# Performance work log

Measured on AMD Instinct MI355X. Metric: run time of the kernel, lower is better.

Reference implementation:

```python
import jax, jax.numpy as jnp
import numpy as np

EMBED_DIM_LIST = [256, 512]
NUM_HEADS_LIST = [4, 8]
MAX_EMBED = 512
N_BASE = 8                       # = max(num_heads_list)
MAX_HS = max(EMBED_DIM_LIST) // min(NUM_HEADS_LIST)  # 128


def _config_masks():
    # One {0,1} mask per (emb, heads) config, shape [n_cfg, N_BASE, MAX_HS, MAX_EMBED].
    # Mask encodes: slice base weight [:head_size, :emb], zero-pad to (MAX_HS, MAX_EMBED),
    # and that only the first `heads` base heads receive a contribution.
    r = np.arange(MAX_HS)[:, None]
    c = np.arange(MAX_EMBED)[None, :]
    masks = []
    for emb in EMBED_DIM_LIST:
        for heads in NUM_HEADS_LIST:
            hs = emb // heads
            m2 = ((r < hs) & (c < emb)).astype(np.float32)      # [MAX_HS, MAX_EMBED]
            hm = (np.arange(N_BASE) < heads).astype(np.float32)  # [N_BASE]
            masks.append(hm[:, None, None] * m2[None])
    return jnp.asarray(np.stack(masks))  # [4, 8, 128, 512]

_CFG_MASKS = _config_masks()


def setup_inputs() -> dict:
    key = jax.random.key(0)
    k0, k1, k2, k3, k4 = jax.random.split(key, 5)
    B, T = 4, 2048
    x = jax.random.normal(k0, (B, T, MAX_EMBED), dtype=jnp.float32)
    weights = jax.random.uniform(k1, (len(EMBED_DIM_LIST) * len(NUM_HEADS_LIST),), dtype=jnp.float32)
    s = 0.02
    base_K = jax.random.normal(k2, (N_BASE, MAX_HS, MAX_EMBED), dtype=jnp.float32) * s
    base_Q = jax.random.normal(k3, (N_BASE, MAX_HS, MAX_EMBED), dtype=jnp.float32) * s
    base_V = jax.random.normal(k4, (N_BASE, MAX_HS, MAX_EMBED), dtype=jnp.float32) * s
    return {"x": x, "weights": weights, "base_K": base_K, "base_Q": base_Q, "base_V": base_V}


def reference(x, weights, base_K, base_Q, base_V):
    B, T, C = x.shape
    # Weight mixing: sum_i weights[i] * (padded slice of base weight) for each base head.
    eff = jnp.einsum('i,ihde->hde', weights, _CFG_MASKS)  # [H, MAX_HS, MAX_EMBED]
    Wk = eff * base_K
    Wq = eff * base_Q
    Wv = eff * base_V
    # Projections for all base heads at once: F.linear(x, W) == x @ W.T
    k = jnp.einsum('btc,hdc->bhtd', x, Wk)
    q = jnp.einsum('btc,hdc->bhtd', x, Wq)
    v = jnp.einsum('btc,hdc->bhtd', x, Wv)
    # Causal self-attention; scale uses k.shape[-1] == MAX_HS (padded head size), as in source.
    scale = 1.0 / jnp.sqrt(jnp.asarray(MAX_HS, dtype=x.dtype))
    att = jnp.einsum('bhtd,bhsd->bhts', q, k) * scale       # [B, H, T, T]
    tril = jnp.tril(jnp.ones((T, T), dtype=bool))
    att = jnp.where(tril, att, -jnp.inf)
    wei = jax.nn.softmax(att, axis=-1)                       # dropout = identity (eval)
    out = jnp.einsum('bhts,bhsd->bhtd', wei, v)              # [B, H, T, MAX_HS]
    # torch.cat(head_out_list, dim=-1) in head order == transpose + reshape
    return out.transpose(0, 2, 1, 3).reshape(B, T, N_BASE * MAX_HS)
```

## Files before the change

### kernel.cpp

```cpp
#include <hip/hip_runtime.h>
#include <hip/hip_bf16.h>
#include <stdint.h>

typedef __attribute__((ext_vector_type(8))) short bf16x8;
typedef __attribute__((ext_vector_type(4))) float f32x4;
typedef __attribute__((ext_vector_type(16))) float f32x16;

#define MFMA16(a,b,c) __builtin_amdgcn_mfma_f32_16x16x32_bf16((a),(b),(c),0,0,0)
#define MFMA32(a,b,c) __builtin_amdgcn_mfma_f32_32x32x16_bf16((a),(b),(c),0,0,0)
#define AS1 __attribute__((address_space(1)))
#define AS3 __attribute__((address_space(3)))

__device__ inline short f2bf(float f) {
    union { __hip_bfloat16 h; short s; } u;
    u.h = __float2bfloat16(f);
    return u.s;
}
__device__ inline uint32_t pack_bf16(float a, float b) {
    union { __hip_bfloat16 h; uint16_t u; } ua, ub;
    ua.h = __float2bfloat16(a); ub.h = __float2bfloat16(b);
    return (uint32_t)ua.u | ((uint32_t)ub.u << 16);
}

#if __has_builtin(__builtin_amdgcn_permlane32_swap)
#define SWAP32(x, y, a, b) { auto _r = __builtin_amdgcn_permlane32_swap((a),(b),false,false); \
                             (x) = _r[0]; (y) = _r[1]; }
#else
#define SWAP32(x, y, a, b) { uint32_t _ta = __shfl_xor((uint32_t)(a),32); \
                             uint32_t _tb = __shfl_xor((uint32_t)(b),32); \
                             (x) = hh_ ? _tb : (a); (y) = hh_ ? (b) : _ta; }
#endif

#define QSCALE 0.12751879523879295f

#define NW (8*128*512)
#define NWC (768*512)
#define NX4 (8192*512/4)
#define NZ1 262144

__global__ void prep_kernel(const float* __restrict__ x,
                            const float* __restrict__ w,
                            const float* __restrict__ bK,
                            const float* __restrict__ bQ,
                            const float* __restrict__ bV,
                            short* __restrict__ xb,
                            short* __restrict__ W,
                            short* __restrict__ qkv)
{
    const float w0 = w[0], w1 = w[1], w2 = w[2], w3 = w[3];
    const size_t HSTRIDE = (size_t)2048 * 128;
    const uint4 zz = {0u, 0u, 0u, 0u};
    for (int i = blockIdx.x * blockDim.x + threadIdx.x; i < NW + NX4 + 3 * NZ1;
         i += gridDim.x * blockDim.x) {
        if (i < NW) {
            int e = i & 511;
            int d = (i >> 9) & 127;
            int h = i >> 16;
            if (h >= 4 && d >= 64) continue;
            float eff = 0.f;
            if (h < 4) { eff += w2; if (d < 64 && e < 256) eff += w0; }
            if (d < 32 && e < 256) eff += w1;
            if (d < 64) eff += w3;
            int r = (h < 4) ? (h * 128 + d) : (512 + (h - 4) * 64 + d);
            int idx = r * 512 + e;
            W[idx]           = f2bf(eff * bK[i]);
            W[idx + NWC]     = f2bf(eff * bQ[i] * QSCALE);
            W[idx + 2*NWC]   = f2bf(eff * bV[i]);
        } else if (i < NW + NX4) {
            int j = i - NW;
            float4 v = ((const float4*)x)[j];
            short4 o;
            o.x = f2bf(v.x); o.y = f2bf(v.y); o.z = f2bf(v.z); o.w = f2bf(v.w);
            ((short4*)xb)[j] = o;
        } else {
            int z = i - NW - NX4;
            int reg = z / NZ1;
            int zz_ = z - reg * NZ1;
            int bhidx = zz_ >> 14;
            int rem = zz_ & 16383;
            int bh = (bhidx >> 2) * 8 + 4 + (bhidx & 3);
            short* p;
            if (reg < 2) {
                int t = rem >> 3, ch = rem & 7;
                p = qkv + (size_t)reg * 32 * HSTRIDE + (size_t)bh * HSTRIDE
                    + (size_t)t * 128 + 64 + ch * 8;
            } else {
                p = qkv + (size_t)64 * HSTRIDE + (size_t)bh * HSTRIDE
                    + (size_t)64 * 2048 + (size_t)rem * 8;
            }
            *(uint4*)p = zz;
        }
    }
}

__global__ __launch_bounds__(256)
void proj_gemm(const short* __restrict__ A,
               const short* __restrict__ Bw,
               short* __restrict__ qkv)
{
    __shared__ short S[128 * 128];
    short* As = S;
    short* Bs = S + 128 * 64;
    const int tid = threadIdx.x;
    const int lane = tid & 63;
    const int wave = tid >> 6;
    const int wr = wave >> 1, wc = wave & 1;
    const int l15 = lane & 15, lk = lane >> 4;

    const int wg = (blockIdx.x & 7) * 144 + (blockIdx.x >> 3);
    const int bm = (wg / 18) * 128;
    const int tt = wg % 18;
    const int bn = tt * 128;
    const int p = tt / 6;
    const int u = tt % 6;

    char* Ab = (char*)As;
    char* Bb = (char*)Bs;
    char* Sb = (char*)S;
    f32x4 acc[4][4] = {};

    for (int k0 = 0; k0 < 512; k0 += 64) {
        __syncthreads();
#pragma unroll
        for (int i = 0; i < 4; ++i) {
            int c = i * 256 + tid;
            int lin = c * 16;
            int row = lin >> 7;
            int cof = ((lin & 127) ^ ((row & 7) << 4)) >> 1;
            __builtin_amdgcn_global_load_lds(
                (const AS1 void*)(A + (size_t)(bm + row) * 512 + k0 + cof),
                (AS3 void*)(As + c * 8), 16, 0, 0);
            __builtin_amdgcn_global_load_lds(
                (const AS1 void*)(Bw + (size_t)(bn + row) * 512 + k0 + cof),
                (AS3 void*)(Bs + c * 8), 16, 0, 0);
        }
        __syncthreads();
#pragma unroll
        for (int kk = 0; kk < 2; ++kk) {
            bf16x8 af[4], bfv[4];
#pragma unroll
            for (int mi = 0; mi < 4; ++mi) {
                int row = wr * 64 + mi * 16 + l15;
                af[mi] = *(const bf16x8*)(Ab + ((row * 128 + kk * 64 + lk * 16) ^ ((row & 7) << 4)));
            }
#pragma unroll
            for (int ni = 0; ni < 4; ++ni) {
                int row = wc * 64 + ni * 16 + l15;
                bfv[ni] = *(const bf16x8*)(Bb + ((row * 128 + kk * 64 + lk * 16) ^ ((row & 7) << 4)));
            }
#pragma unroll
            for (int mi = 0; mi < 4; ++mi)
#pragma unroll
                for (int ni = 0; ni < 4; ++ni)
                    acc[mi][ni] = MFMA16(af[mi], bfv[ni], acc[mi][ni]);
        }
    }

    const int b = bm >> 11;
    const int tbase = bm & 2047;

    __syncthreads();
    if (p == 2) {
#pragma unroll
        for (int mi = 0; mi < 4; ++mi) {
#pragma unroll
            for (int ni = 0; ni < 4; ++ni) {
                int dl = wc * 64 + ni * 16 + l15;
                int tlb = wr * 64 + mi * 16 + lk * 4;
                int byte0 = (dl * 256 + tlb * 2) ^ ((dl & 7) << 4);
                *(uint32_t*)(Sb + byte0)     = pack_bf16(acc[mi][ni][0], acc[mi][ni][1]);
                *(uint32_t*)(Sb + byte0 + 4) = pack_bf16(acc[mi][ni][2], acc[mi][ni][3]);
            }
        }
    } else {
#pragma unroll
        for (int mi = 0; mi < 4; ++mi) {
#pragma unroll
            for (int ni = 0; ni < 4; ++ni) {
                int dl = wc * 64 + ni * 16 + l15;
#pragma unroll
                for (int r = 0; r < 4; ++r) {
                    int tl = wr * 64 + mi * 16 + lk * 4 + r;
                    *(short*)(Sb + ((tl * 256 + dl * 2) ^ ((tl & 7) << 4))) = f2bf(acc[mi][ni][r]);
                }
            }
        }
    }
    __syncthreads();

#pragma unroll
    for (int i = 0; i < 8; ++i) {
        int c = i * 256 + tid;
        int row = c >> 4;
        uint4 v = *(const uint4*)(Sb + row * 256 + (((c & 15) * 16) ^ ((row & 7) << 4)));
        if (p == 2) {
            int head, drow;
            if (u < 4) { head = u;                         drow = row;      }
            else       { head = 4 + (u - 4) * 2 + (row >> 6); drow = row & 63; }
            short* dst = qkv + (size_t)2 * (32 * 2048 * 128)
                       + (size_t)(b * 8 + head) * 128 * 2048;
            *(uint4*)(dst + (size_t)drow * 2048 + tbase + (c & 15) * 8) = v;
        } else {
            int cc = c & 15;
            int head, dcol;
            if (u < 4) { head = u;                          dcol = cc * 8;       }
            else       { head = 4 + (u - 4) * 2 + (cc >> 3); dcol = (cc & 7) * 8; }
            short* dst = qkv + (size_t)p * (32 * 2048 * 128)
                       + (size_t)(b * 8 + head) * 2048 * 128;
            *(uint4*)(dst + (size_t)(tbase + row) * 128 + dcol) = v;
        }
    }
}

__global__ __launch_bounds__(512, 2)
void attn_kernel(const short* __restrict__ qkv, float* __restrict__ out)
{
    extern __shared__ char smem[];
    const int tid = threadIdx.x, lane = tid & 63, wave = tid >> 6;
    const int l31 = lane & 31;
    const int hh_ = lane >> 5;

    const int bh = blockIdx.x & 31;
    const int a = blockIdx.x >> 5;

    const int qc = wave & 3;
    const int kvh = wave >> 2;

    const size_t HSTRIDE = (size_t)2048 * 128;
    const short* Kp = qkv + (size_t)bh * HSTRIDE;
    const short* Qp = qkv + (size_t)32 * HSTRIDE + (size_t)bh * HSTRIDE;
    const short* Vp = qkv + (size_t)64 * HSTRIDE + (size_t)bh * HSTRIDE;

    int koffs[4], voffs[4];
#pragma unroll
    for (int i = 0; i < 4; ++i) {
        int c = i * 512 + tid;
        int rk = c >> 4;
        int kof = (((c * 16) & 255) ^ ((rk & 15) << 4)) >> 1;
        koffs[i] = rk * 128 + kof;
        int sub = c >> 10, cc = c & 1023;
        int rv = cc >> 4;
        int pp = ((cc * 16) & 255) ^ ((rv & 15) << 4);
        int d = 2 * rv + (pp >> 7);
        int t = (pp & 127) >> 1;
        voffs[i] = d * 2048 + sub * 64 + t;
    }

#define STAGE128(J0, BUF) {                                                   \
        char* _b = smem + ((BUF) << 16);                                      \
        _Pragma("unroll")                                                     \
        for (int i = 0; i < 4; ++i) {                                         \
            int c = i * 512 + tid;                                            \
            __builtin_amdgcn_global_load_lds(                                 \
                (const AS1 void*)(Kp + koffs[i] + (J0) * 128),                \
                (AS3 void*)(_b + c * 16), 16, 0, 0);                          \
            __builtin_amdgcn_global_load_lds(                                 \
                (const AS1 void*)(Vp + voffs[i] + (J0)),                      \
                (AS3 void*)(_b + 32768 + c * 16), 16, 0, 0);                  \
        }                                                                     \
    }

    for (int sidx = 0; sidx < 2; ++sidx) {
        const int sp = sidx ? (15 - a) : a;
        const int q0 = sp * 128;
        const int nt = sp + 1;
        const int qwave = q0 + qc * 32;
        const int qglob = qwave + l31;

        __syncthreads();

        bf16x8 qf[8];
        {
            const short* qrow = Qp + (size_t)(q0 + qc * 32 + l31) * 128 + hh_ * 8;
#pragma unroll
            for (int dblk = 0; dblk < 8; ++dblk)
                qf[dblk] = *(const bf16x8*)(qrow + dblk * 16);
        }

        float mrow = -1e30f, lrow = 0.f;
        f32x16 acco[4] = {};

        STAGE128(0, 0);
        asm volatile("s_waitcnt vmcnt(0)" ::: "memory");
        __builtin_amdgcn_sched_barrier(0);
        __builtin_amdgcn_s_barrier();
        __builtin_amdgcn_sched_barrier(0);

        for (int jt = 0; jt < nt; ++jt) {
            const int j0 = jt << 7;
            if (jt + 1 < nt)
                STAGE128((jt + 1) << 7, (jt + 1) & 1);

            const int kv0 = j0 + kvh * 64;
            if (kv0 <= qwave + 31) {
                const char* Kb = smem + ((jt & 1) << 16);
                const char* Vb = Kb + 32768 + (kvh << 14);

                f32x16 sacc[2] = {};
                __builtin_amdgcn_s_setprio(1);
#pragma unroll
                for (int dblk = 0; dblk < 8; ++dblk) {
#pragma unroll
                    for (int kvt = 0; kvt < 2; ++kvt) {
                        int krow = kvh * 64 + kvt * 32 + l31;
                        bf16x8 kf = *(const bf16x8*)(Kb + krow * 256 +
                            ((dblk * 32 + hh_ * 16) ^ ((krow & 15) << 4)));
                        sacc[kvt] = MFMA32(kf, qf[dblk], sacc[kvt]);
                    }
                }
                __builtin_amdgcn_s_setprio(0);

                if (kv0 + 63 > qwave) {
#pragma unroll
                    for (int kvt = 0; kvt < 2; ++kvt)
#pragma unroll
                        for (int r = 0; r < 16; ++r) {
                            int kvglob = kv0 + kvt * 32 + (r & 3) + 8 * (r >> 2) + 4 * hh_;
                            if (kvglob > qglob) sacc[kvt][r] = -1e30f;
                        }
                }

                float pmax = -1e30f;
#pragma unroll
                for (int kvt = 0; kvt < 2; ++kvt)
#pragma unroll
                    for (int r = 0; r < 16; r += 4) {
                        float a2 = fmaxf(sacc[kvt][r], sacc[kvt][r + 1]);
                        float b2 = fmaxf(sacc[kvt][r + 2], sacc[kvt][r + 3]);
                        pmax = fmaxf(pmax, fmaxf(a2, b2));
                    }
                pmax = fmaxf(pmax, __shfl_xor(pmax, 32));

                if (!__all(pmax - mrow <= 11.5416f)) {
                    float mn = fmaxf(mrow, pmax);
                    float alpha = __builtin_amdgcn_exp2f(mrow - mn);
                    mrow = mn;
                    lrow *= alpha;
#pragma unroll
                    for (int r = 0; r < 16; ++r) {
                        float ar = __shfl(alpha, (r & 3) + 8 * (r >> 2) + 4 * hh_);
#pragma unroll
                        for (int dt = 0; dt < 4; ++dt) acco[dt][r] *= ar;
                    }
                }

                float psum = 0.f;
                uint32_t pkA[2][4], pkB[2][4];
#pragma unroll
                for (int kvt = 0; kvt < 2; ++kvt)
#pragma unroll
                    for (int sg = 0; sg < 4; ++sg) {
                        float p0 = __builtin_amdgcn_exp2f(sacc[kvt][4 * sg + 0] - mrow);
                        float p1 = __builtin_amdgcn_exp2f(sacc[kvt][4 * sg + 1] - mrow);
                        float p2 = __builtin_amdgcn_exp2f(sacc[kvt][4 * sg + 2] - mrow);
                        float p3 = __builtin_amdgcn_exp2f(sacc[kvt][4 * sg + 3] - mrow);
                        psum += (p0 + p1) + (p2 + p3);
                        pkA[kvt][sg] = pack_bf16(p0, p1);
                        pkB[kvt][sg] = pack_bf16(p2, p3);
                    }
                psum += __shfl_xor(psum, 32);
                lrow += psum;

                __builtin_amdgcn_s_setprio(1);
#pragma unroll
                for (int w = 0; w < 4; ++w) {
                    const int kvt = w >> 1, kbl = w & 1;
                    uint32_t r0, r1, r2, r3;
                    SWAP32(r0, r2, pkA[kvt][2 * kbl], pkA[kvt][2 * kbl + 1]);
                    SWAP32(r1, r3, pkB[kvt][2 * kbl], pkB[kvt][2 * kbl + 1]);
                    union { uint32_t u[4]; bf16x8 v; } pa;
                    pa.u[0] = r0; pa.u[1] = r1; pa.u[2] = r2; pa.u[3] = r3;
#pragma unroll
                    for (int dt = 0; dt < 4; ++dt) {
                        int d = dt * 32 + l31;
                        int r = d >> 1;
                        int inner = ((d & 1) << 7) + w * 32 + hh_ * 16;
                        bf16x8 vf = *(const bf16x8*)(Vb + r * 256 + (inner ^ ((r & 15) << 4)));
                        acco[dt] = MFMA32(pa.v, vf, acco[dt]);
                    }
                }
                __builtin_amdgcn_s_setprio(0);
            }

            if (jt + 1 < nt) {
                asm volatile("s_waitcnt vmcnt(0)" ::: "memory");
                __builtin_amdgcn_sched_barrier(0);
                __builtin_amdgcn_s_barrier();
                __builtin_amdgcn_sched_barrier(0);
            }
        }

        __syncthreads();
        float* ex = (float*)smem;
        float* ml = (float*)(smem + 65536);
        if (kvh == 1) {
            float* dst = ex + qc * 4096;
#pragma unroll
            for (int dt = 0; dt < 4; ++dt)
#pragma unroll
                for (int r = 0; r < 16; ++r)
                    dst[(dt * 16 + r) * 64 + lane] = acco[dt][r];
            ml[qc * 128 + lane * 2 + 0] = mrow;
            ml[qc * 128 + lane * 2 + 1] = lrow;
        }
        __syncthreads();
        if (kvh == 0) {
            float m1 = ml[qc * 128 + lane * 2 + 0];
            float l1 = ml[qc * 128 + lane * 2 + 1];
            float M  = fmaxf(mrow, m1);
            float av = __builtin_amdgcn_exp2f(mrow - M);
            float bv = __builtin_amdgcn_exp2f(m1 - M);
            float lf = lrow * av + l1 * bv;
            float sA = av / lf, sB = bv / lf;
            const float* src = ex + qc * 4096;
            const int bb = bh >> 3, hd = bh & 7;
#pragma unroll
            for (int r = 0; r < 16; ++r) {
                int ql = (r & 3) + 8 * (r >> 2) + 4 * hh_;
                float sa = __shfl(sA, ql);
                float sb = __shfl(sB, ql);
                int t = qwave + ql;
                float* o = out + (size_t)(bb * 2048 + t) * 1024 + hd * 128 + l31;
#pragma unroll
                for (int dt = 0; dt < 4; ++dt)
                    o[dt * 32] = acco[dt][r] * sa + src[(dt * 16 + r) * 64 + lane] * sb;
            }
        }
        asm volatile("s_waitcnt vmcnt(0)" ::: "memory");
    }
#undef STAGE128
}

extern "C" void kernel_launch(void* const* d_in, const int* in_sizes, int n_in,
                              void* d_out, int out_size, void* d_ws, size_t ws_size,
                              hipStream_t stream) {
    const float* x  = (const float*)d_in[0];
    const float* w  = (const float*)d_in[1];
    const float* bK = (const float*)d_in[2];
    const float* bQ = (const float*)d_in[3];
    const float* bV = (const float*)d_in[4];

    short* xb  = (short*)d_ws;
    short* W   = (short*)((char*)d_ws + 8388608);
    short* qkv = (short*)((char*)d_ws + 8388608 + 3145728);
    float* out = (float*)d_out;

    hipFuncSetAttribute((const void*)attn_kernel,
                        hipFuncAttributeMaxDynamicSharedMemorySize, 131072);

    prep_kernel<<<2048, 256, 0, stream>>>(x, w, bK, bQ, bV, xb, W, qkv);
    proj_gemm<<<64 * 18, 256, 0, stream>>>(xb, W, qkv);
    attn_kernel<<<256, 512, 131072, stream>>>(qkv, out);
}
```

Baseline: 99.65 us.

## Skip zero-padded V/Q loads for small heads and hoist V LDS reads

```diff
diff --git a/kernel.cpp b/kernel.cpp
--- a/kernel.cpp
+++ b/kernel.cpp
@@ -36,7 +36,7 @@
 #define NW (8*128*512)
 #define NWC (768*512)
 #define NX4 (8192*512/4)
-#define NZ1 262144
+#define NZK 262144
 
 __global__ void prep_kernel(const float* __restrict__ x,
                             const float* __restrict__ w,
@@ -49,8 +49,8 @@
 {
     const float w0 = w[0], w1 = w[1], w2 = w[2], w3 = w[3];
     const size_t HSTRIDE = (size_t)2048 * 128;
-    const uint4 zz = {0u, 0u, 0u, 0u};
-    for (int i = blockIdx.x * blockDim.x + threadIdx.x; i < NW + NX4 + 3 * NZ1;
+    const uint4 z4 = {0u, 0u, 0u, 0u};
+    for (int i = blockIdx.x * blockDim.x + threadIdx.x; i < NW + NX4 + NZK;
          i += gridDim.x * blockDim.x) {
         if (i < NW) {
             int e = i & 511;
@@ -74,21 +74,12 @@
             ((short4*)xb)[j] = o;
         } else {
             int z = i - NW - NX4;
-            int reg = z / NZ1;
-            int zz_ = z - reg * NZ1;
-            int bhidx = zz_ >> 14;
-            int rem = zz_ & 16383;
+            int bhidx = z >> 14;
+            int rem = z & 16383;
             int bh = (bhidx >> 2) * 8 + 4 + (bhidx & 3);
-            short* p;
-            if (reg < 2) {
-                int t = rem >> 3, ch = rem & 7;
-                p = qkv + (size_t)reg * 32 * HSTRIDE + (size_t)bh * HSTRIDE
-                    + (size_t)t * 128 + 64 + ch * 8;
-            } else {
-                p = qkv + (size_t)64 * HSTRIDE + (size_t)bh * HSTRIDE
-                    + (size_t)64 * 2048 + (size_t)rem * 8;
-            }
-            *(uint4*)p = zz;
+            int t = rem >> 3, ch = rem & 7;
+            short* p = qkv + (size_t)bh * HSTRIDE + (size_t)t * 128 + 64 + ch * 8;
+            *(uint4*)p = z4;
         }
     }
 }
@@ -222,6 +213,7 @@
 
     const int bh = blockIdx.x & 31;
     const int a = blockIdx.x >> 5;
+    const bool zh = ((bh & 7) >= 4);
 
     const int qc = wave & 3;
     const int kvh = wave >> 2;
@@ -249,14 +241,15 @@
 #define STAGE128(J0, BUF) {                                                   \
         char* _b = smem + ((BUF) << 16);                                      \
         _Pragma("unroll")                                                     \
-        for (int i = 0; i < 4; ++i) {                                         \
-            int c = i * 512 + tid;                                            \
+        for (int i_ = 0; i_ < 4; ++i_) {                                      \
+            int c = i_ * 512 + tid;                                           \
             __builtin_amdgcn_global_load_lds(                                 \
-                (const AS1 void*)(Kp + koffs[i] + (J0) * 128),                \
+                (const AS1 void*)(Kp + koffs[i_] + (J0) * 128),               \
                 (AS3 void*)(_b + c * 16), 16, 0, 0);                          \
-            __builtin_amdgcn_global_load_lds(                                 \
-                (const AS1 void*)(Vp + voffs[i] + (J0)),                      \
-                (AS3 void*)(_b + 32768 + c * 16), 16, 0, 0);                  \
+            if (!zh || !(i_ & 1))                                             \
+                __builtin_amdgcn_global_load_lds(                             \
+                    (const AS1 void*)(Vp + voffs[i_] + (J0)),                 \
+                    (AS3 void*)(_b + 32768 + c * 16), 16, 0, 0);              \
         }                                                                     \
     }
 
@@ -269,12 +262,34 @@
 
         __syncthreads();
 
+        if (zh) {
+            const uint4 z4 = {0u, 0u, 0u, 0u};
+#pragma unroll
+            for (int bq = 0; bq < 2; ++bq) {
+                char* _b = smem + (bq << 16);
+#pragma unroll
+                for (int i2 = 1; i2 < 4; i2 += 2) {
+                    int c = i2 * 512 + tid;
+                    *(uint4*)(_b + 32768 + c * 16) = z4;
+                }
+            }
+            __syncthreads();
+        }
+
         bf16x8 qf[8];
         {
             const short* qrow = Qp + (size_t)(q0 + qc * 32 + l31) * 128 + hh_ * 8;
-#pragma unroll
-            for (int dblk = 0; dblk < 8; ++dblk)
+            const bf16x8 zerov = {};
+#pragma unroll
+            for (int dblk = 0; dblk < 4; ++dblk)
                 qf[dblk] = *(const bf16x8*)(qrow + dblk * 16);
+            if (zh) {
+                qf[4] = zerov; qf[5] = zerov; qf[6] = zerov; qf[7] = zerov;
+            } else {
+#pragma unroll
+                for (int dblk = 4; dblk < 8; ++dblk)
+                    qf[dblk] = *(const bf16x8*)(qrow + dblk * 16);
+            }
         }
 
         float mrow = -1e30f, lrow = 0.f;
@@ -310,6 +325,18 @@
                 }
                 __builtin_amdgcn_s_setprio(0);
 
+                bf16x8 vf[4][4];
+#pragma unroll
+                for (int w = 0; w < 4; ++w) {
+#pragma unroll
+                    for (int dt = 0; dt < 4; ++dt) {
+                        int d = dt * 32 + l31;
+                        int r = d >> 1;
+                        int inner = ((d & 1) << 7) + w * 32 + hh_ * 16;
+                        vf[w][dt] = *(const bf16x8*)(Vb + r * 256 + (inner ^ ((r & 15) << 4)));
+                    }
+                }
+
                 if (kv0 + 63 > qwave) {
 #pragma unroll
                     for (int kvt = 0; kvt < 2; ++kvt)
@@ -329,7 +356,12 @@
                         float b2 = fmaxf(sacc[kvt][r + 2], sacc[kvt][r + 3]);
                         pmax = fmaxf(pmax, fmaxf(a2, b2));
                     }
-                pmax = fmaxf(pmax, __shfl_xor(pmax, 32));
+                {
+                    uint32_t pa_ = __builtin_bit_cast(uint32_t, pmax), xx_, yy_;
+                    SWAP32(xx_, yy_, pa_, pa_);
+                    pmax = fmaxf(__builtin_bit_cast(float, xx_),
+                                 __builtin_bit_cast(float, yy_));
+                }
 
                 if (!__all(pmax - mrow <= 11.5416f)) {
                     float mn = fmaxf(mrow, pmax);
@@ -358,7 +390,12 @@
                         pkA[kvt][sg] = pack_bf16(p0, p1);
                         pkB[kvt][sg] = pack_bf16(p2, p3);
                     }
-                psum += __shfl_xor(psum, 32);
+                {
+                    uint32_t pa_ = __builtin_bit_cast(uint32_t, psum), xx_, yy_;
+                    SWAP32(xx_, yy_, pa_, pa_);
+                    psum = __builtin_bit_cast(float, xx_) +
+                           __builtin_bit_cast(float, yy_);
+                }
                 lrow += psum;
 
                 __builtin_amdgcn_s_setprio(1);
@@ -371,13 +408,8 @@
                     union { uint32_t u[4]; bf16x8 v; } pa;
                     pa.u[0] = r0; pa.u[1] = r1; pa.u[2] = r2; pa.u[3] = r3;
 #pragma unroll
-                    for (int dt = 0; dt < 4; ++dt) {
-                        int d = dt * 32 + l31;
-                        int r = d >> 1;
-                        int inner = ((d & 1) << 7) + w * 32 + hh_ * 16;
-                        bf16x8 vf = *(const bf16x8*)(Vb + r * 256 + (inner ^ ((r & 15) << 4)));
-                        acco[dt] = MFMA32(pa.v, vf, acco[dt]);
-                    }
+                    for (int dt = 0; dt < 4; ++dt)
+                        acco[dt] = MFMA32(pa.v, vf[w][dt], acco[dt]);
                 }
                 __builtin_amdgcn_s_setprio(0);
             }
```

Result: no change. 100.4 us (+0.8%).
